# Kernel optimization log

Measured on AMD Instinct MI355X. Metric: run time of the kernel, lower is better.

The kernel has to match this reference:

```python
import jax, jax.numpy as jnp
import numpy as np

DIM = 512
HEADS = 8
HEAD_DIM = DIM // HEADS
SCALE = HEAD_DIM ** -0.5
EPS = 1e-5


def setup_inputs() -> dict:
    key = jax.random.key(0)
    ks = jax.random.split(key, 6)
    B, N, C = 4, 2048, DIM
    x = jax.random.normal(ks[0], (B, N, C), dtype=jnp.float32)
    w_qkv = jax.random.normal(ks[1], (C, 3 * C), dtype=jnp.float32) * (C ** -0.5)
    w_proj = jax.random.normal(ks[2], (C, C), dtype=jnp.float32) * (C ** -0.5)
    b_proj = jax.random.normal(ks[3], (C,), dtype=jnp.float32) * 0.02
    gamma = jnp.ones((C,), dtype=jnp.float32)
    beta = jnp.zeros((C,), dtype=jnp.float32)
    return {"x": x, "w_qkv": w_qkv, "w_proj": w_proj, "b_proj": b_proj,
            "gamma": gamma, "beta": beta}


def reference(x, w_qkv, w_proj, b_proj, gamma, beta):
    B, N, C = x.shape
    # LayerNorm over channel dim
    mu = jnp.mean(x, axis=-1, keepdims=True)
    var = jnp.mean(jnp.square(x - mu), axis=-1, keepdims=True)
    xn = (x - mu) * jax.lax.rsqrt(var + EPS) * gamma + beta
    # QKV projection (fp32, no bias)
    qkv = xn @ w_qkv  # [B, N, 3C]
    qkv = qkv.reshape(B, N, 3, HEADS, HEAD_DIM)
    q = jnp.transpose(qkv[:, :, 0], (0, 2, 1, 3))  # [B, H, N, D]
    k = jnp.transpose(qkv[:, :, 1], (0, 2, 1, 3))
    v = jnp.transpose(qkv[:, :, 2], (0, 2, 1, 3))
    attn = jnp.einsum('bhnd,bhmd->bhnm', q, k) * SCALE
    attn = jax.nn.softmax(attn, axis=-1)
    out = jnp.einsum('bhnm,bhmd->bhnd', attn, v)  # [B, H, N, D]
    out = jnp.transpose(out, (0, 2, 1, 3)).reshape(B, N, C)
    out = out @ w_proj + b_proj
    return x + out
```

## Files before the change

### kernel.cpp

```cpp
#include <hip/hip_runtime.h>
#include <hip/hip_bf16.h>
#include <math.h>

typedef _Float16 f16;
typedef _Float16 half8 __attribute__((ext_vector_type(8)));
typedef _Float16 half4 __attribute__((ext_vector_type(4)));
typedef float f32x4 __attribute__((ext_vector_type(4)));

#define DIMC 512
#define HEADS 8
#define HD 64
#define BB 4
#define NN 2048
#define MM (BB*NN)
#define NQKV (3*DIMC)
#define SCALE 0.125f
#define LOG2E 1.44269504f
#define EPSLN 1e-5f

__device__ __forceinline__ void g2l16(const void* g, void* l) {
    __builtin_amdgcn_global_load_lds(
        (const __attribute__((address_space(1))) unsigned int*)g,
        (__attribute__((address_space(3))) unsigned int*)l, 16, 0, 0);
}

__global__ __launch_bounds__(256) void ln_kernel(const float* __restrict__ x,
                                                 const float* __restrict__ gamma,
                                                 const float* __restrict__ beta,
                                                 f16* __restrict__ xn) {
    int w = threadIdx.x >> 6;
    int lane = threadIdx.x & 63;
    int row = blockIdx.x * 4 + w;
    const float* xr = x + (size_t)row * DIMC;
    float4 v0 = ((const float4*)xr)[lane * 2];
    float4 v1 = ((const float4*)xr)[lane * 2 + 1];
    float s = v0.x + v0.y + v0.z + v0.w + v1.x + v1.y + v1.z + v1.w;
#pragma unroll
    for (int off = 1; off < 64; off <<= 1) s += __shfl_xor(s, off);
    float mu = s * (1.0f / DIMC);
    float d0 = v0.x - mu, d1 = v0.y - mu, d2 = v0.z - mu, d3 = v0.w - mu;
    float d4 = v1.x - mu, d5 = v1.y - mu, d6 = v1.z - mu, d7 = v1.w - mu;
    float s2 = d0*d0 + d1*d1 + d2*d2 + d3*d3 + d4*d4 + d5*d5 + d6*d6 + d7*d7;
#pragma unroll
    for (int off = 1; off < 64; off <<= 1) s2 += __shfl_xor(s2, off);
    float rstd = rsqrtf(s2 * (1.0f / DIMC) + EPSLN);
    float4 g0 = ((const float4*)gamma)[lane * 2];
    float4 g1 = ((const float4*)gamma)[lane * 2 + 1];
    float4 b0 = ((const float4*)beta)[lane * 2];
    float4 b1 = ((const float4*)beta)[lane * 2 + 1];
    half8 o;
    o[0] = (f16)(d0 * rstd * g0.x + b0.x);
    o[1] = (f16)(d1 * rstd * g0.y + b0.y);
    o[2] = (f16)(d2 * rstd * g0.z + b0.z);
    o[3] = (f16)(d3 * rstd * g0.w + b0.w);
    o[4] = (f16)(d4 * rstd * g1.x + b1.x);
    o[5] = (f16)(d5 * rstd * g1.y + b1.y);
    o[6] = (f16)(d6 * rstd * g1.z + b1.z);
    o[7] = (f16)(d7 * rstd * g1.w + b1.w);
    ((half8*)(xn + (size_t)row * DIMC))[lane] = o;
}

__global__ __launch_bounds__(256) void transpose_cast(const float* __restrict__ src,
                                                      f16* __restrict__ dst,
                                                      int R, int C) {
    __shared__ f16 t[32][72];
    int k0 = blockIdx.y * 32, n0 = blockIdx.x * 64;
    int tid = threadIdx.x;
    int rr = tid >> 6, col = tid & 63;
#pragma unroll
    for (int p = 0; p < 8; p++) {
        int r = p * 4 + rr;
        t[r][col] = (f16)src[(size_t)(k0 + r) * C + n0 + col];
    }
    __syncthreads();
    int nl = tid >> 2, kc = (tid & 3) * 8;
    half8 v;
#pragma unroll
    for (int j = 0; j < 8; j++) v[j] = t[kc + j][nl];
    *(half8*)&dst[(size_t)(n0 + nl) * R + k0 + kc] = v;
}

__device__ __forceinline__ void gemm128_loop(const char* Ag, const char* Bg,
                                             f16* As, f16* Bs, f32x4 (&acc)[4][4]) {
    int tid = threadIdx.x;
    int w = tid >> 6, lane = tid & 63, l15 = lane & 15, quad = lane >> 4;
    int wy = w >> 1, wx = w & 1;
    int off0 = w * 1024 + lane * 16;
    for (int kk = 0; kk < 16; ++kk) {
        __syncthreads();
#pragma unroll
        for (int c = 0; c < 2; ++c) {
            int off = c * 4096 + off0;
            int row = off >> 6, col = off & 63;
            g2l16(Ag + (size_t)row * 1024 + kk * 64 + col, (char*)As + c * 4096 + w * 1024);
            g2l16(Bg + (size_t)row * 1024 + kk * 64 + col, (char*)Bs + c * 4096 + w * 1024);
        }
        __syncthreads();
        half8 af[4], bf[4];
#pragma unroll
        for (int i = 0; i < 4; ++i) {
            af[i] = *(const half8*)((const char*)As + ((wy * 64 + i * 16 + l15) << 6) + quad * 16);
            bf[i] = *(const half8*)((const char*)Bs + ((wx * 64 + i * 16 + l15) << 6) + quad * 16);
        }
#pragma unroll
        for (int i = 0; i < 4; ++i)
#pragma unroll
            for (int j = 0; j < 4; ++j)
                acc[i][j] = __builtin_amdgcn_mfma_f32_16x16x32_f16(af[i], bf[j], acc[i][j], 0, 0, 0);
    }
}

__global__ __launch_bounds__(256) void gemm_qkv(const f16* __restrict__ xn,
                                                const f16* __restrict__ wt,
                                                f16* __restrict__ qb,
                                                f16* __restrict__ kbuf,
                                                f16* __restrict__ vtb) {
    __shared__ __align__(16) f16 As[128 * 32];
    __shared__ __align__(16) f16 Bs[128 * 32];
    int tid = threadIdx.x;
    int w = tid >> 6, lane = tid & 63, l15 = lane & 15, quad = lane >> 4;
    int wy = w >> 1, wx = w & 1;
    int m0 = blockIdx.y * 128, c0 = blockIdx.x * 128;
    f32x4 acc[4][4] = {};
    gemm128_loop((const char*)(xn + (size_t)m0 * DIMC),
                 (const char*)(wt + (size_t)c0 * DIMC), As, Bs, acc);
    int bx = blockIdx.x;
    if (bx < 8) {
        const float QS = SCALE * LOG2E;
        f16* dst = (bx < 4) ? qb : kbuf;
        float mul = (bx < 4) ? QS : 1.0f;
        int cb = (bx < 4) ? c0 : c0 - DIMC;
#pragma unroll
        for (int i = 0; i < 4; ++i)
#pragma unroll
            for (int j = 0; j < 4; ++j)
#pragma unroll
                for (int r = 0; r < 4; ++r) {
                    int m = m0 + wy * 64 + i * 16 + quad * 4 + r;
                    int c = cb + wx * 64 + j * 16 + l15;
                    int b = m >> 11, n = m & 2047;
                    int h = c >> 6, d = c & 63;
                    dst[(((size_t)(b * HEADS + h)) * NN + n) * HD + d] = (f16)(acc[i][j][r] * mul);
                }
    } else {
        __syncthreads();
        f16* T = (f16*)As + w * 512;
        int cb = c0 - 2 * DIMC;
        int dl = lane >> 2, mp = lane & 3;
#pragma unroll
        for (int i = 0; i < 4; ++i)
#pragma unroll
            for (int j = 0; j < 4; ++j) {
                half4 hv;
#pragma unroll
                for (int r = 0; r < 4; ++r) hv[r] = (f16)acc[i][j][r];
                *(half4*)&T[l15 * 20 + quad * 4] = hv;
                half4 rv = *(half4*)&T[dl * 20 + mp * 4];
                int c = cb + wx * 64 + j * 16 + dl;
                int m = m0 + wy * 64 + i * 16 + mp * 4;
                int b = m >> 11, n = m & 2047;
                int h = c >> 6, d = c & 63;
                *(half4*)&vtb[(((size_t)(b * HEADS + h)) * HD + d) * NN + n] = rv;
            }
    }
}

__global__ __launch_bounds__(256, 4) void attn_kernel(const f16* __restrict__ qb,
                                                      const f16* __restrict__ kbuf,
                                                      const f16* __restrict__ vtb,
                                                      f16* __restrict__ po,
                                                      float2* __restrict__ pml) {
    __shared__ __align__(16) f16 Ks[64 * 72];
    __shared__ __align__(16) f16 Vs[64 * 72];
    __shared__ __align__(16) f16 Ps[4][32 * 72];
    int bh = blockIdx.y;
    int chunk = blockIdx.z;
    int n0 = blockIdx.x * 128;
    int tid = threadIdx.x, w = tid >> 6, lane = tid & 63, l15 = lane & 15, quad = lane >> 4;
    const f16* Kbase = kbuf + (size_t)bh * NN * HD;
    const f16* Vbase = vtb + (size_t)bh * HD * NN;
    const f16* Qbase = qb + (size_t)bh * NN * HD;
    half8 qf[2][2];
#pragma unroll
    for (int qt = 0; qt < 2; ++qt) {
        const f16* qr = Qbase + (size_t)(n0 + w * 32 + qt * 16 + l15) * HD + quad * 8;
        qf[qt][0] = *(const half8*)qr;
        qf[qt][1] = *(const half8*)(qr + 32);
    }
    f32x4 o[2][4] = {};
    f32x4 lacc[2] = {};
    float m_run[2] = {-INFINITY, -INFINITY};
    int srow = tid >> 2, part = (tid & 3) * 16;
    int kbeg = chunk * (NN / 2);
    half8 ones;
#pragma unroll
    for (int j = 0; j < 8; ++j) ones[j] = (f16)1.0f;
    half8 kp0, kp1, vp0, vp1;
    {
        const f16* kg = Kbase + (size_t)(kbeg + srow) * HD + part;
        kp0 = ((const half8*)kg)[0]; kp1 = ((const half8*)kg)[1];
        const f16* vg = Vbase + (size_t)srow * NN + kbeg + part;
        vp0 = ((const half8*)vg)[0]; vp1 = ((const half8*)vg)[1];
    }
    for (int it = 0; it < 16; ++it) {
        __syncthreads();
        *(half8*)&Ks[srow * 72 + part] = kp0;
        *(half8*)&Ks[srow * 72 + part + 8] = kp1;
        *(half8*)&Vs[srow * 72 + part] = vp0;
        *(half8*)&Vs[srow * 72 + part + 8] = vp1;
        __syncthreads();
        if (it < 15) {
            int kt0 = kbeg + (it + 1) * 64;
            const f16* kg = Kbase + (size_t)(kt0 + srow) * HD + part;
            kp0 = ((const half8*)kg)[0]; kp1 = ((const half8*)kg)[1];
            const f16* vg = Vbase + (size_t)srow * NN + kt0 + part;
            vp0 = ((const half8*)vg)[0]; vp1 = ((const half8*)vg)[1];
        }
        f32x4 s0[4], s1[4];
#pragma unroll
        for (int kt = 0; kt < 4; ++kt) {
            half8 a0 = *(const half8*)&Ks[(kt * 16 + l15) * 72 + quad * 8];
            half8 a1 = *(const half8*)&Ks[(kt * 16 + l15) * 72 + 32 + quad * 8];
            f32x4 z0 = {};
            z0 = __builtin_amdgcn_mfma_f32_16x16x32_f16(a0, qf[0][0], z0, 0, 0, 0);
            z0 = __builtin_amdgcn_mfma_f32_16x16x32_f16(a1, qf[0][1], z0, 0, 0, 0);
            s0[kt] = z0;
            f32x4 z1 = {};
            z1 = __builtin_amdgcn_mfma_f32_16x16x32_f16(a0, qf[1][0], z1, 0, 0, 0);
            z1 = __builtin_amdgcn_mfma_f32_16x16x32_f16(a1, qf[1][1], z1, 0, 0, 0);
            s1[kt] = z1;
        }
#pragma unroll
        for (int qt = 0; qt < 2; ++qt) {
            f32x4* s = (qt == 0) ? s0 : s1;
            float tmax = -INFINITY;
#pragma unroll
            for (int kt = 0; kt < 4; ++kt)
#pragma unroll
                for (int r = 0; r < 4; ++r) tmax = fmaxf(tmax, s[kt][r]);
            tmax = fmaxf(tmax, __shfl_xor(tmax, 16));
            tmax = fmaxf(tmax, __shfl_xor(tmax, 32));
            float m_new = fmaxf(m_run[qt], tmax);
            float alpha = __builtin_amdgcn_exp2f(m_run[qt] - m_new);
            m_run[qt] = m_new;
#pragma unroll
            for (int kt = 0; kt < 4; ++kt)
#pragma unroll
                for (int r = 0; r < 4; ++r)
                    s[kt][r] = __builtin_amdgcn_exp2f(s[kt][r] - m_new);
            float ar[4];
#pragma unroll
            for (int r = 0; r < 4; ++r) ar[r] = __shfl(alpha, quad * 4 + r);
#pragma unroll
            for (int nt = 0; nt < 4; ++nt)
#pragma unroll
                for (int r = 0; r < 4; ++r) o[qt][nt][r] *= ar[r];
#pragma unroll
            for (int r = 0; r < 4; ++r) lacc[qt][r] *= ar[r];
            f16* P = &Ps[w][(qt * 16 + l15) * 72];
#pragma unroll
            for (int kt = 0; kt < 4; ++kt) {
                half4 pk;
#pragma unroll
                for (int r = 0; r < 4; ++r) pk[r] = (f16)s[kt][r];
                *(half4*)&P[kt * 16 + quad * 4] = pk;
            }
        }
#pragma unroll
        for (int qt = 0; qt < 2; ++qt) {
            half8 pa0 = *(const half8*)&Ps[w][(qt * 16 + l15) * 72 + quad * 8];
            half8 pa1 = *(const half8*)&Ps[w][(qt * 16 + l15) * 72 + 32 + quad * 8];
            lacc[qt] = __builtin_amdgcn_mfma_f32_16x16x32_f16(pa0, ones, lacc[qt], 0, 0, 0);
            lacc[qt] = __builtin_amdgcn_mfma_f32_16x16x32_f16(pa1, ones, lacc[qt], 0, 0, 0);
#pragma unroll
            for (int nt = 0; nt < 4; ++nt) {
                half8 vb0 = *(const half8*)&Vs[(nt * 16 + l15) * 72 + quad * 8];
                half8 vb1 = *(const half8*)&Vs[(nt * 16 + l15) * 72 + 32 + quad * 8];
                o[qt][nt] = __builtin_amdgcn_mfma_f32_16x16x32_f16(pa0, vb0, o[qt][nt], 0, 0, 0);
                o[qt][nt] = __builtin_amdgcn_mfma_f32_16x16x32_f16(pa1, vb1, o[qt][nt], 0, 0, 0);
            }
        }
    }
    size_t rowbase = ((size_t)chunk * (BB * HEADS) + bh) * NN;
#pragma unroll
    for (int qt = 0; qt < 2; ++qt) {
        int qrow = n0 + w * 32 + qt * 16;
        if (quad == 0) pml[rowbase + qrow + l15].x = m_run[qt];
        if (l15 == 0) {
#pragma unroll
            for (int r = 0; r < 4; ++r)
                pml[rowbase + qrow + quad * 4 + r].y = lacc[qt][r];
        }
#pragma unroll
        for (int nt = 0; nt < 4; ++nt)
#pragma unroll
            for (int r = 0; r < 4; ++r) {
                int n = qrow + quad * 4 + r;
                po[(rowbase + n) * HD + nt * 16 + l15] = (f16)o[qt][nt][r];
            }
    }
}

__global__ __launch_bounds__(256) void attn_combine(const f16* __restrict__ po,
                                                    const float2* __restrict__ pml,
                                                    f16* __restrict__ ao) {
    int gid = blockIdx.x * 256 + threadIdx.x;
    int row = gid >> 3, d0 = (gid & 7) * 8;
    int bh = row >> 11, n = row & 2047;
    const int CS = BB * HEADS * NN;
    float2 ml1 = pml[row];
    float2 ml2 = pml[row + CS];
    half8 o1 = *(const half8*)&po[(size_t)row * HD + d0];
    half8 o2 = *(const half8*)&po[((size_t)row + CS) * HD + d0];
    float M = fmaxf(ml1.x, ml2.x);
    float a1 = __builtin_amdgcn_exp2f(ml1.x - M);
    float a2 = __builtin_amdgcn_exp2f(ml2.x - M);
    float inv = 1.0f / (ml1.y * a1 + ml2.y * a2);
    a1 *= inv; a2 *= inv;
    half8 r;
#pragma unroll
    for (int j = 0; j < 8; ++j) r[j] = (f16)((float)o1[j] * a1 + (float)o2[j] * a2);
    int h = bh & 7, b = bh >> 3;
    *(half8*)&ao[((size_t)(b * NN + n)) * DIMC + h * HD + d0] = r;
}

__global__ __launch_bounds__(256) void gemm_proj(const f16* __restrict__ aob,
                                                 const f16* __restrict__ wt,
                                                 const float* __restrict__ x,
                                                 const float* __restrict__ bias,
                                                 float* __restrict__ out) {
    __shared__ __align__(16) f16 As[128 * 32];
    __shared__ __align__(16) f16 Bs[64 * 32];
    int tid = threadIdx.x;
    int w = tid >> 6, lane = tid & 63, l15 = lane & 15, quad = lane >> 4;
    int m0 = blockIdx.y * 128, c0 = blockIdx.x * 64;
    const char* Ag = (const char*)(aob + (size_t)m0 * DIMC);
    const char* Bg = (const char*)(wt + (size_t)c0 * DIMC);
    f32x4 acc[2][4] = {};
    int off0 = w * 1024 + lane * 16;
    for (int kk = 0; kk < 16; ++kk) {
        __syncthreads();
#pragma unroll
        for (int c = 0; c < 2; ++c) {
            int off = c * 4096 + off0;
            int row = off >> 6, col = off & 63;
            g2l16(Ag + (size_t)row * 1024 + kk * 64 + col, (char*)As + c * 4096 + w * 1024);
        }
        {
            int off = tid * 16;
            int row = off >> 6, col = off & 63;
            g2l16(Bg + (size_t)row * 1024 + kk * 64 + col, (char*)Bs + w * 1024);
        }
        __syncthreads();
        half8 af[2], bf[4];
#pragma unroll
        for (int i = 0; i < 2; ++i)
            af[i] = *(const half8*)((const char*)As + ((w * 32 + i * 16 + l15) << 6) + quad * 16);
#pragma unroll
        for (int j = 0; j < 4; ++j)
            bf[j] = *(const half8*)((const char*)Bs + ((j * 16 + l15) << 6) + quad * 16);
#pragma unroll
        for (int i = 0; i < 2; ++i)
#pragma unroll
            for (int j = 0; j < 4; ++j)
                acc[i][j] = __builtin_amdgcn_mfma_f32_16x16x32_f16(af[i], bf[j], acc[i][j], 0, 0, 0);
    }
#pragma unroll
    for (int i = 0; i < 2; ++i)
#pragma unroll
        for (int j = 0; j < 4; ++j)
#pragma unroll
            for (int r = 0; r < 4; ++r) {
                int m = m0 + w * 32 + i * 16 + quad * 4 + r;
                int c = c0 + j * 16 + l15;
                out[(size_t)m * DIMC + c] = x[(size_t)m * DIMC + c] + bias[c] + acc[i][j][r];
            }
}

extern "C" void kernel_launch(void* const* d_in, const int* in_sizes, int n_in,
                              void* d_out, int out_size, void* d_ws, size_t ws_size,
                              hipStream_t stream) {
    (void)in_sizes; (void)n_in; (void)out_size; (void)ws_size;
    const float* x     = (const float*)d_in[0];
    const float* wqkv  = (const float*)d_in[1];
    const float* wproj = (const float*)d_in[2];
    const float* bproj = (const float*)d_in[3];
    const float* gamma = (const float*)d_in[4];
    const float* beta  = (const float*)d_in[5];
    float* out = (float*)d_out;

    char* ws = (char*)d_ws;
    f16* xn     = (f16*)ws;                 ws += (size_t)MM * DIMC * 2;
    f16* wqkvt  = (f16*)ws;                 ws += (size_t)NQKV * DIMC * 2;
    f16* wprojt = (f16*)ws;                 ws += (size_t)DIMC * DIMC * 2;
    f16* qbuf   = (f16*)ws;                 ws += (size_t)MM * DIMC * 2;
    f16* kbuf   = (f16*)ws;                 ws += (size_t)MM * DIMC * 2;
    f16* vtbuf  = (f16*)ws;                 ws += (size_t)MM * DIMC * 2;
    f16* aobuf  = (f16*)ws;                 ws += (size_t)MM * DIMC * 2;
    f16* po     = (f16*)ws;                 ws += (size_t)2 * BB * HEADS * NN * HD * 2;
    float2* pml = (float2*)ws;              ws += (size_t)2 * BB * HEADS * NN * sizeof(float2);

    ln_kernel<<<MM / 4, 256, 0, stream>>>(x, gamma, beta, xn);
    transpose_cast<<<dim3(NQKV / 64, DIMC / 32), 256, 0, stream>>>(wqkv, wqkvt, DIMC, NQKV);
    transpose_cast<<<dim3(DIMC / 64, DIMC / 32), 256, 0, stream>>>(wproj, wprojt, DIMC, DIMC);
    gemm_qkv<<<dim3(NQKV / 128, MM / 128), 256, 0, stream>>>(xn, wqkvt, qbuf, kbuf, vtbuf);
    attn_kernel<<<dim3(NN / 128, BB * HEADS, 2), 256, 0, stream>>>(qbuf, kbuf, vtbuf, po, pml);
    attn_combine<<<(BB * HEADS * NN * HD / 8) / 256, 256, 0, stream>>>(po, pml, aobuf);
    gemm_proj<<<dim3(DIMC / 64, MM / 128), 256, 0, stream>>>(aobuf, wprojt, x, bproj, out);
}
```

Measured before the change: 185.2 us.

## Keep P in registers via transposed PV MFMA and split keys into four chunks

```diff
diff --git a/kernel.cpp b/kernel.cpp
--- a/kernel.cpp
+++ b/kernel.cpp
@@ -17,6 +17,7 @@
 #define SCALE 0.125f
 #define LOG2E 1.44269504f
 #define EPSLN 1e-5f
+#define NCHUNK 4
 
 __device__ __forceinline__ void g2l16(const void* g, void* l) {
     __builtin_amdgcn_global_load_lds(
@@ -172,7 +173,6 @@
                                                       float2* __restrict__ pml) {
     __shared__ __align__(16) f16 Ks[64 * 72];
     __shared__ __align__(16) f16 Vs[64 * 72];
-    __shared__ __align__(16) f16 Ps[4][32 * 72];
     int bh = blockIdx.y;
     int chunk = blockIdx.z;
     int n0 = blockIdx.x * 128;
@@ -187,14 +187,11 @@
         qf[qt][0] = *(const half8*)qr;
         qf[qt][1] = *(const half8*)(qr + 32);
     }
-    f32x4 o[2][4] = {};
-    f32x4 lacc[2] = {};
+    f32x4 ot[2][4] = {};
     float m_run[2] = {-INFINITY, -INFINITY};
+    float l_run[2] = {0.f, 0.f};
     int srow = tid >> 2, part = (tid & 3) * 16;
-    int kbeg = chunk * (NN / 2);
-    half8 ones;
-#pragma unroll
-    for (int j = 0; j < 8; ++j) ones[j] = (f16)1.0f;
+    int kbeg = chunk * (NN / NCHUNK);
     half8 kp0, kp1, vp0, vp1;
     {
         const f16* kg = Kbase + (size_t)(kbeg + srow) * HD + part;
@@ -202,14 +199,14 @@
         const f16* vg = Vbase + (size_t)srow * NN + kbeg + part;
         vp0 = ((const half8*)vg)[0]; vp1 = ((const half8*)vg)[1];
     }
-    for (int it = 0; it < 16; ++it) {
+    for (int it = 0; it < NN / NCHUNK / 64; ++it) {
         __syncthreads();
         *(half8*)&Ks[srow * 72 + part] = kp0;
         *(half8*)&Ks[srow * 72 + part + 8] = kp1;
         *(half8*)&Vs[srow * 72 + part] = vp0;
         *(half8*)&Vs[srow * 72 + part + 8] = vp1;
         __syncthreads();
-        if (it < 15) {
+        if (it < NN / NCHUNK / 64 - 1) {
             int kt0 = kbeg + (it + 1) * 64;
             const f16* kg = Kbase + (size_t)(kt0 + srow) * HD + part;
             kp0 = ((const half8*)kg)[0]; kp1 = ((const half8*)kg)[1];
@@ -230,6 +227,7 @@
             z1 = __builtin_amdgcn_mfma_f32_16x16x32_f16(a1, qf[1][1], z1, 0, 0, 0);
             s1[kt] = z1;
         }
+        half4 pb[2][4];
 #pragma unroll
         for (int qt = 0; qt < 2; ++qt) {
             f32x4* s = (qt == 0) ? s0 : s1;
@@ -243,61 +241,54 @@
             float m_new = fmaxf(m_run[qt], tmax);
             float alpha = __builtin_amdgcn_exp2f(m_run[qt] - m_new);
             m_run[qt] = m_new;
+            float lsum = 0.f;
 #pragma unroll
             for (int kt = 0; kt < 4; ++kt)
 #pragma unroll
-                for (int r = 0; r < 4; ++r)
-                    s[kt][r] = __builtin_amdgcn_exp2f(s[kt][r] - m_new);
-            float ar[4];
-#pragma unroll
-            for (int r = 0; r < 4; ++r) ar[r] = __shfl(alpha, quad * 4 + r);
-#pragma unroll
-            for (int nt = 0; nt < 4; ++nt)
-#pragma unroll
-                for (int r = 0; r < 4; ++r) o[qt][nt][r] *= ar[r];
-#pragma unroll
-            for (int r = 0; r < 4; ++r) lacc[qt][r] *= ar[r];
-            f16* P = &Ps[w][(qt * 16 + l15) * 72];
+                for (int r = 0; r < 4; ++r) {
+                    float p = __builtin_amdgcn_exp2f(s[kt][r] - m_new);
+                    s[kt][r] = p;
+                    lsum += p;
+                }
+            lsum += __shfl_xor(lsum, 16);
+            lsum += __shfl_xor(lsum, 32);
+            l_run[qt] = l_run[qt] * alpha + lsum;
+#pragma unroll
+            for (int dt = 0; dt < 4; ++dt)
+#pragma unroll
+                for (int r = 0; r < 4; ++r) ot[qt][dt][r] *= alpha;
 #pragma unroll
             for (int kt = 0; kt < 4; ++kt) {
                 half4 pk;
 #pragma unroll
                 for (int r = 0; r < 4; ++r) pk[r] = (f16)s[kt][r];
-                *(half4*)&P[kt * 16 + quad * 4] = pk;
+                pb[qt][kt] = pk;
             }
         }
 #pragma unroll
-        for (int qt = 0; qt < 2; ++qt) {
-            half8 pa0 = *(const half8*)&Ps[w][(qt * 16 + l15) * 72 + quad * 8];
-            half8 pa1 = *(const half8*)&Ps[w][(qt * 16 + l15) * 72 + 32 + quad * 8];
-            lacc[qt] = __builtin_amdgcn_mfma_f32_16x16x32_f16(pa0, ones, lacc[qt], 0, 0, 0);
-            lacc[qt] = __builtin_amdgcn_mfma_f32_16x16x32_f16(pa1, ones, lacc[qt], 0, 0, 0);
-#pragma unroll
-            for (int nt = 0; nt < 4; ++nt) {
-                half8 vb0 = *(const half8*)&Vs[(nt * 16 + l15) * 72 + quad * 8];
-                half8 vb1 = *(const half8*)&Vs[(nt * 16 + l15) * 72 + 32 + quad * 8];
-                o[qt][nt] = __builtin_amdgcn_mfma_f32_16x16x32_f16(pa0, vb0, o[qt][nt], 0, 0, 0);
-                o[qt][nt] = __builtin_amdgcn_mfma_f32_16x16x32_f16(pa1, vb1, o[qt][nt], 0, 0, 0);
+        for (int kt = 0; kt < 4; ++kt)
+#pragma unroll
+            for (int dt = 0; dt < 4; ++dt) {
+                half4 av = *(const half4*)&Vs[(dt * 16 + l15) * 72 + kt * 16 + quad * 4];
+                ot[0][dt] = __builtin_amdgcn_mfma_f32_16x16x16f16(av, pb[0][kt], ot[0][dt], 0, 0, 0);
+                ot[1][dt] = __builtin_amdgcn_mfma_f32_16x16x16f16(av, pb[1][kt], ot[1][dt], 0, 0, 0);
             }
-        }
     }
     size_t rowbase = ((size_t)chunk * (BB * HEADS) + bh) * NN;
 #pragma unroll
     for (int qt = 0; qt < 2; ++qt) {
-        int qrow = n0 + w * 32 + qt * 16;
-        if (quad == 0) pml[rowbase + qrow + l15].x = m_run[qt];
-        if (l15 == 0) {
-#pragma unroll
-            for (int r = 0; r < 4; ++r)
-                pml[rowbase + qrow + quad * 4 + r].y = lacc[qt][r];
-        }
-#pragma unroll
-        for (int nt = 0; nt < 4; ++nt)
-#pragma unroll
-            for (int r = 0; r < 4; ++r) {
-                int n = qrow + quad * 4 + r;
-                po[(rowbase + n) * HD + nt * 16 + l15] = (f16)o[qt][nt][r];
-            }
+        int n = n0 + w * 32 + qt * 16 + l15;
+        if (quad == 0) {
+            float2 ml; ml.x = m_run[qt]; ml.y = l_run[qt];
+            pml[rowbase + n] = ml;
+        }
+#pragma unroll
+        for (int dt = 0; dt < 4; ++dt) {
+            half4 hv;
+#pragma unroll
+            for (int r = 0; r < 4; ++r) hv[r] = (f16)ot[qt][dt][r];
+            *(half4*)&po[(rowbase + n) * HD + dt * 16 + quad * 4] = hv;
+        }
     }
 }
 
@@ -308,18 +299,30 @@
     int row = gid >> 3, d0 = (gid & 7) * 8;
     int bh = row >> 11, n = row & 2047;
     const int CS = BB * HEADS * NN;
-    float2 ml1 = pml[row];
-    float2 ml2 = pml[row + CS];
-    half8 o1 = *(const half8*)&po[(size_t)row * HD + d0];
-    half8 o2 = *(const half8*)&po[((size_t)row + CS) * HD + d0];
-    float M = fmaxf(ml1.x, ml2.x);
-    float a1 = __builtin_amdgcn_exp2f(ml1.x - M);
-    float a2 = __builtin_amdgcn_exp2f(ml2.x - M);
-    float inv = 1.0f / (ml1.y * a1 + ml2.y * a2);
-    a1 *= inv; a2 *= inv;
+    float2 ml[NCHUNK];
+    float M = -INFINITY;
+#pragma unroll
+    for (int c = 0; c < NCHUNK; ++c) {
+        ml[c] = pml[row + c * CS];
+        M = fmaxf(M, ml[c].x);
+    }
+    float a[NCHUNK], denom = 0.f;
+#pragma unroll
+    for (int c = 0; c < NCHUNK; ++c) {
+        a[c] = __builtin_amdgcn_exp2f(ml[c].x - M);
+        denom += ml[c].y * a[c];
+    }
+    float inv = 1.0f / denom;
+    float acc[8] = {};
+#pragma unroll
+    for (int c = 0; c < NCHUNK; ++c) {
+        half8 oc = *(const half8*)&po[((size_t)row + c * CS) * HD + d0];
+#pragma unroll
+        for (int j = 0; j < 8; ++j) acc[j] += (float)oc[j] * a[c];
+    }
     half8 r;
 #pragma unroll
-    for (int j = 0; j < 8; ++j) r[j] = (f16)((float)o1[j] * a1 + (float)o2[j] * a2);
+    for (int j = 0; j < 8; ++j) r[j] = (f16)(acc[j] * inv);
     int h = bh & 7, b = bh >> 3;
     *(half8*)&ao[((size_t)(b * NN + n)) * DIMC + h * HD + d0] = r;
 }
@@ -397,14 +400,14 @@
     f16* kbuf   = (f16*)ws;                 ws += (size_t)MM * DIMC * 2;
     f16* vtbuf  = (f16*)ws;                 ws += (size_t)MM * DIMC * 2;
     f16* aobuf  = (f16*)ws;                 ws += (size_t)MM * DIMC * 2;
-    f16* po     = (f16*)ws;                 ws += (size_t)2 * BB * HEADS * NN * HD * 2;
-    float2* pml = (float2*)ws;              ws += (size_t)2 * BB * HEADS * NN * sizeof(float2);
+    f16* po     = (f16*)ws;                 ws += (size_t)NCHUNK * BB * HEADS * NN * HD * 2;
+    float2* pml = (float2*)ws;              ws += (size_t)NCHUNK * BB * HEADS * NN * sizeof(float2);
 
     ln_kernel<<<MM / 4, 256, 0, stream>>>(x, gamma, beta, xn);
     transpose_cast<<<dim3(NQKV / 64, DIMC / 32), 256, 0, stream>>>(wqkv, wqkvt, DIMC, NQKV);
     transpose_cast<<<dim3(DIMC / 64, DIMC / 32), 256, 0, stream>>>(wproj, wprojt, DIMC, DIMC);
     gemm_qkv<<<dim3(NQKV / 128, MM / 128), 256, 0, stream>>>(xn, wqkvt, qbuf, kbuf, vtbuf);
-    attn_kernel<<<dim3(NN / 128, BB * HEADS, 2), 256, 0, stream>>>(qbuf, kbuf, vtbuf, po, pml);
+    attn_kernel<<<dim3(NN / 128, BB * HEADS, NCHUNK), 256, 0, stream>>>(qbuf, kbuf, vtbuf, po, pml);
     attn_combine<<<(BB * HEADS * NN * HD / 8) / 256, 256, 0, stream>>>(po, pml, aobuf);
     gemm_proj<<<dim3(DIMC / 64, MM / 128), 256, 0, stream>>>(aobuf, wprojt, x, bproj, out);
 }
```

Measured after the change: 184.8 us. No clear change (-0.2%).
